# Performance work log

Hardware: AMD Instinct MI355X
Metric: run time of the kernel (lower is better)

Reference implementation:

```python
import jax, jax.numpy as jnp
import numpy as np

B_SZ, L_SEQ, H_CH, N_ST = 8, 4096, 256, 64


def setup_inputs() -> dict:
    key = jax.random.key(0)
    ks = jax.random.split(key, 12)
    rn = lambda k, s, sc=1.0: jax.random.normal(k, s, jnp.float32) * sc
    inp = {
        'x': rn(ks[0], (B_SZ, L_SEQ, H_CH)),
        # stable DPLR spectrum: Re(Lambda) < 0, HiPPO-like imaginary ladder
        'Lambda_re': -(jnp.abs(rn(ks[1], (N_ST,))) + 0.1),
        'Lambda_im': jnp.pi * jnp.arange(N_ST, dtype=jnp.float32),
        'P_re': rn(ks[2], (N_ST,), N_ST ** -0.5),
        'P_im': rn(ks[3], (N_ST,), N_ST ** -0.5),
        'Q_re': rn(ks[4], (N_ST,), N_ST ** -0.5),
        'Q_im': rn(ks[5], (N_ST,), N_ST ** -0.5),
        'B_re': rn(ks[6], (N_ST,), N_ST ** -0.5),
        'B_im': rn(ks[7], (N_ST,), N_ST ** -0.5),
        'C_re': rn(ks[8], (H_CH, N_ST), N_ST ** -0.5),
        'C_im': rn(ks[9], (H_CH, N_ST), N_ST ** -0.5),
        'step': jnp.ones((1,), jnp.float32) * 1e-3,
        'D': jnp.zeros((1,), jnp.float32),
        'W_fc': rn(ks[10], (H_CH, H_CH), H_CH ** -0.5),
        'b_fc': jnp.zeros((H_CH,), jnp.float32),
        'ln_g': jnp.ones((H_CH,), jnp.float32),
        'ln_b': jnp.zeros((H_CH,), jnp.float32),
    }
    return inp


def _dplr_kernel(Lambda_re, Lambda_im, P_re, P_im, Q_re, Q_im, B_re, B_im, C_re, C_im, step, L):
    # S4 DPLR generating function evaluated at the L roots of unity (torch_get_K_derta).
    Lam = (Lambda_re + 1j * Lambda_im).astype(jnp.complex64)  # (N,)
    Pc = (P_re + 1j * P_im).astype(jnp.complex64)
    Qc = (Q_re + 1j * Q_im).astype(jnp.complex64)
    Bc = (B_re + 1j * B_im).astype(jnp.complex64)
    Cc = (C_re + 1j * C_im).astype(jnp.complex64)  # (H, N)
    k = jnp.arange(L, dtype=jnp.float32)
    Omega = jnp.exp((-2j * jnp.pi) * (k / L)).astype(jnp.complex64)  # (L,)
    c = 2.0 / (1.0 + Omega)
    g = (2.0 / step[0]) * (1.0 - Omega) / (1.0 + Omega)  # bilinear transform points, (L,)
    inv = 1.0 / (g[:, None] - Lam[None, :])  # Cauchy matrix, (L, N)
    k00 = jnp.einsum('hn,ln->hl', Cc * Bc[None, :], inv)  # (H, L)
    k01 = jnp.einsum('hn,ln->hl', Cc * Pc[None, :], inv)
    k10 = jnp.einsum('n,ln->l', Qc * Bc, inv)  # (L,)
    k11 = jnp.einsum('n,ln->l', Qc * Pc, inv)
    atRoots = c[None, :] * (k00 - k01 * (k10 / (1.0 + k11))[None, :])  # Woodbury correction
    K = jnp.fft.ifft(atRoots, axis=-1).real  # (H, L)
    return K.astype(jnp.float32)


def reference(x, Lambda_re, Lambda_im, P_re, P_im, Q_re, Q_im, B_re, B_im, C_re, C_im, step, D, W_fc, b_fc, ln_g, ln_b):
    Bsz, L, H = x.shape
    step = jnp.maximum(step, 1e-6)
    K = _dplr_kernel(Lambda_re, Lambda_im, P_re, P_im, Q_re, Q_im, B_re, B_im, C_re, C_im, step, L)  # (H, L)
    # causal FFT convolution per channel (torch_convolution with fft=True)
    n = 2 * L
    Kf = jnp.fft.rfft(K, n=n, axis=-1)           # (H, F)
    uf = jnp.fft.rfft(x, n=n, axis=1)            # (B, F, H)
    h1 = jnp.fft.irfft(uf * Kf.T[None], n=n, axis=1)[:, :L, :]
    y1 = jax.nn.gelu(h1 + D * x, approximate=False)  # mult_activation='gelu'
    y2 = jax.nn.gelu(y1 @ W_fc.T + b_fc, approximate=False)  # fc + final_act
    y2 = y2 + x  # skip
    mu = jnp.mean(y2, axis=-1, keepdims=True)
    var = jnp.var(y2, axis=-1, keepdims=True)
    y = (y2 - mu) / jnp.sqrt(var + 1e-5) * ln_g + ln_b  # LayerNorm; dropout p=0
    h_ratio = jnp.max(jnp.abs(y), axis=1) / (jnp.max(jnp.abs(x), axis=1) + 1e-6)  # (B, H)
    return y, h_ratio
```

## Files before the change

### kernel.cpp

```cpp
#include <hip/hip_runtime.h>
#include <math.h>

#define TPB 256

typedef float2 cf;
typedef __attribute__((ext_vector_type(8))) short bf16x8;
typedef __attribute__((ext_vector_type(4))) float f32x4;

__device__ __forceinline__ cf cmk(float x, float y){ cf r; r.x=x; r.y=y; return r; }
__device__ __forceinline__ cf cml(cf a, cf b){ return cmk(a.x*b.x - a.y*b.y, a.x*b.y + a.y*b.x); }
__device__ __forceinline__ cf cad(cf a, cf b){ return cmk(a.x+b.x, a.y+b.y); }
__device__ __forceinline__ cf csb(cf a, cf b){ return cmk(a.x-b.x, a.y-b.y); }
__device__ __forceinline__ cf crcp(cf d){ float r = 1.0f/(d.x*d.x + d.y*d.y); return cmk(d.x*r, -d.y*r); }
__device__ __forceinline__ cf cdv(cf n, cf d){ return cml(n, crcp(d)); }
__device__ __forceinline__ float geluf(float z){ return 0.5f*z*(1.0f + erff(z*0.70710678118654752f)); }

__device__ __forceinline__ cf twid(float f, float sign){
  float h = f * 0.5f;
  float s = __builtin_amdgcn_sinf(h);
  float c0 = __builtin_amdgcn_cosf(h);
  return cmk(c0, sign * s);
}

__device__ __forceinline__ void bfsplit(float v, ushort* h, ushort* l){
  unsigned u = __float_as_uint(v);
  unsigned hr = (u + 0x7FFFu + ((u >> 16) & 1u)) & 0xFFFF0000u;
  *h = (ushort)(hr >> 16);
  float lv = v - __uint_as_float(hr);
  unsigned u2 = __float_as_uint(lv);
  *l = (ushort)((u2 + 0x7FFFu + ((u2 >> 16) & 1u)) >> 16);
}

template<int N, int SSTART>
__device__ void fft_dif_r4(cf* __restrict__ a, float sign){
  #pragma unroll
  for (int s = SSTART; s >= 1; s >>= 2){
    __syncthreads();
    #pragma unroll
    for (int g = 0; g < (N >> 2) / TPB; g++){
      int w = (int)threadIdx.x + g * TPB;
      int j = w & (s - 1);
      int base = ((w & ~(s - 1)) << 2) | j;
      cf A0 = a[base], B0 = a[base + s], C0 = a[base + 2*s], D0 = a[base + 3*s];
      cf w1 = twid((float)j / (float)(2 * s), sign);
      cf w2 = cml(w1, w1);
      cf a1 = cad(A0, C0);
      cf c1 = cml(csb(A0, C0), w1);
      cf b1 = cad(B0, D0);
      cf d1 = cml(csb(B0, D0), cmk(-sign * w1.y, sign * w1.x));
      a[base]         = cad(a1, b1);
      a[base + s]     = cml(csb(a1, b1), w2);
      a[base + 2*s]   = cad(c1, d1);
      a[base + 3*s]   = cml(csb(c1, d1), w2);
    }
  }
  if constexpr ((__builtin_ctz(N) & 1) == 1){
    __syncthreads();
    #pragma unroll
    for (int g = 0; g < (N >> 1) / TPB; g++){
      int w = (int)threadIdx.x + g * TPB;
      int i = w << 1;
      cf u = a[i], v = a[i + 1];
      a[i] = cad(u, v);
      a[i + 1] = csb(u, v);
    }
  }
  __syncthreads();
}

template<int N>
__device__ void fft_dit_r4(cf* __restrict__ a, float sign){
  if constexpr ((__builtin_ctz(N) & 1) == 1){
    __syncthreads();
    #pragma unroll
    for (int g = 0; g < (N >> 1) / TPB; g++){
      int w = (int)threadIdx.x + g * TPB;
      int i = w << 1;
      cf u = a[i], v = a[i + 1];
      a[i] = cad(u, v);
      a[i + 1] = csb(u, v);
    }
  }
  constexpr int S0 = ((__builtin_ctz(N) & 1) == 1) ? 2 : 1;
  #pragma unroll
  for (int s = S0; s <= (N >> 2); s <<= 2){
    __syncthreads();
    #pragma unroll
    for (int g = 0; g < (N >> 2) / TPB; g++){
      int w = (int)threadIdx.x + g * TPB;
      int j = w & (s - 1);
      int base = ((w & ~(s - 1)) << 2) | j;
      cf A0 = a[base], B0 = a[base + s], C0 = a[base + 2*s], D0 = a[base + 3*s];
      cf w1 = twid((float)j / (float)(2 * s), sign);
      cf w2 = cml(w1, w1);
      cf t1 = cml(B0, w2);
      cf a1 = cad(A0, t1), b1 = csb(A0, t1);
      cf t2 = cml(D0, w2);
      cf c1 = cad(C0, t2), d1 = csb(C0, t2);
      cf v1 = cml(c1, w1);
      cf v2 = cml(d1, cmk(-sign * w1.y, sign * w1.x));
      a[base]         = cad(a1, v1);
      a[base + 2*s]   = csb(a1, v1);
      a[base + s]     = cad(b1, v2);
      a[base + 3*s]   = csb(b1, v2);
    }
  }
  __syncthreads();
}

__device__ void dif8192_pad_stage(cf* __restrict__ a, float sign){
  __syncthreads();
  #pragma unroll
  for (int g = 0; g < 8; g++){
    int w = (int)threadIdx.x + g * TPB;
    cf A0 = a[w], B0 = a[w + 2048];
    cf w1 = twid((float)w * (1.0f / 4096.0f), sign);
    cf w2 = cml(w1, w1);
    cf c1 = cml(A0, w1);
    cf d1 = cml(B0, cmk(-sign * w1.y, sign * w1.x));
    a[w]        = cad(A0, B0);
    a[w + 2048] = cml(csb(A0, B0), w2);
    a[w + 4096] = cad(c1, d1);
    a[w + 6144] = cml(csb(c1, d1), w2);
  }
}

__device__ __forceinline__ int brev13(int x){ return (int)(__brev((unsigned)x) >> 19); }

__global__ void k_init(unsigned* xmax, unsigned* ymax){
  int i = blockIdx.x * 256 + threadIdx.x;
  if (i < 2048){ xmax[i] = 0u; ymax[i] = 0u; }
}

__global__ __launch_bounds__(256) void k_transpose_x(const float* __restrict__ x,
                                                     float* __restrict__ xT,
                                                     unsigned* __restrict__ xmax){
  __shared__ float tile[64][65];
  __shared__ float red[64][4];
  int b = blockIdx.z;
  int t0 = blockIdx.x * 64;
  int h0 = blockIdx.y * 64;
  int hc = threadIdx.x & 63, tg = threadIdx.x >> 6;
  float pmax = 0.0f;
  #pragma unroll
  for (int q = 0; q < 16; q++){
    int tr = tg + q * 4;
    float v = x[((size_t)(b * 4096 + t0 + tr)) * 256 + h0 + hc];
    tile[tr][hc] = v;
    pmax = fmaxf(pmax, fabsf(v));
  }
  red[hc][tg] = pmax;
  __syncthreads();
  if (threadIdx.x < 64){
    float m = fmaxf(fmaxf(red[threadIdx.x][0], red[threadIdx.x][1]),
                    fmaxf(red[threadIdx.x][2], red[threadIdx.x][3]));
    atomicMax(&xmax[b * 256 + h0 + threadIdx.x], __float_as_uint(m));
  }
  #pragma unroll
  for (int q = 0; q < 16; q++){
    int hr = tg + q * 4;
    xT[((size_t)(b * 256 + h0 + hr)) * 4096 + t0 + hc] = tile[hc][hr];
  }
}

__global__ void k_wsplit(const float* __restrict__ W, ushort* __restrict__ Wh, ushort* __restrict__ Wl){
  int i = blockIdx.x * 256 + threadIdx.x;
  ushort h, l;
  bfsplit(W[i], &h, &l);
  Wh[i] = h; Wl[i] = l;
}

__global__ __launch_bounds__(256) void k_cauchy(
    const float* __restrict__ Lr, const float* __restrict__ Li,
    const float* __restrict__ Pr, const float* __restrict__ Pi,
    const float* __restrict__ Qr, const float* __restrict__ Qi,
    const float* __restrict__ Br, const float* __restrict__ Bi,
    const float* __restrict__ Cr, const float* __restrict__ Ci,
    const float* __restrict__ stepp, cf* __restrict__ A)
{
  __shared__ cf sLam[64], sB[64], sP[64], sQB[64], sQP[64];
  __shared__ cf sInv[64][16];
  __shared__ cf sWood[16], sC[16], sG[16];
  int tid = threadIdx.x;
  int l0 = blockIdx.x * 16;
  float stepv = fmaxf(stepp[0], 1e-6f);
  if (tid < 64){
    cf lam = cmk(Lr[tid], Li[tid]);
    cf b = cmk(Br[tid], Bi[tid]);
    cf p = cmk(Pr[tid], Pi[tid]);
    cf q = cmk(Qr[tid], Qi[tid]);
    sLam[tid] = lam; sB[tid] = b; sP[tid] = p;
    sQB[tid] = cml(q, b);
    sQP[tid] = cml(q, p);
  }
  __syncthreads();
  if (tid < 16){
    int l = l0 + tid;
    float ang = -6.2831855f * ((float)l * (1.0f / 4096.0f));
    cf Om = cmk(cosf(ang), sinf(ang));
    cf den = cmk(1.0f + Om.x, Om.y);
    cf num = cmk(1.0f - Om.x, -Om.y);
    cf rden = crcp(den);
    sC[tid] = cml(cmk(2.0f, 0.0f), rden);
    cf g = cml(num, rden);
    float sc = 2.0f / stepv;
    sG[tid] = cmk(g.x * sc, g.y * sc);
  }
  __syncthreads();
  for (int it = tid; it < 1024; it += 256){
    int n = it >> 4, ll = it & 15;
    sInv[n][ll] = crcp(csb(sG[ll], sLam[n]));
  }
  __syncthreads();
  if (tid < 16){
    cf k10 = cmk(0,0), k11 = cmk(0,0);
    for (int n = 0; n < 64; n++){
      k10 = cad(k10, cml(sQB[n], sInv[n][tid]));
      k11 = cad(k11, cml(sQP[n], sInv[n][tid]));
    }
    sWood[tid] = cdv(k10, cmk(1.0f + k11.x, k11.y));
  }
  __syncthreads();
  int h = tid;
  cf a0[16], a1[16];
  #pragma unroll
  for (int ll = 0; ll < 16; ll++){ a0[ll] = cmk(0,0); a1[ll] = cmk(0,0); }
  for (int n = 0; n < 64; n++){
    cf cc = cmk(Cr[h * 64 + n], Ci[h * 64 + n]);
    cf cb = cml(cc, sB[n]);
    cf cp = cml(cc, sP[n]);
    #pragma unroll
    for (int ll = 0; ll < 16; ll++){
      cf iv = sInv[n][ll];
      a0[ll] = cad(a0[ll], cml(cb, iv));
      a1[ll] = cad(a1[ll], cml(cp, iv));
    }
  }
  cf* dst = A + (size_t)h * 4096 + l0;
  #pragma unroll
  for (int ll = 0; ll < 16; ll++){
    dst[ll] = cml(sC[ll], csb(a0[ll], cml(a1[ll], sWood[ll])));
  }
}

__global__ __launch_bounds__(256) void k_kf(const cf* __restrict__ A, float4* __restrict__ Sab){
  extern __shared__ cf c[];
  int hp = blockIdx.x, tid = threadIdx.x;
  const cf* a1p = A + (size_t)(2 * hp) * 4096;
  const cf* a2p = a1p + 4096;
  for (int l = tid; l < 4096; l += TPB){
    int r = (int)(__brev((unsigned)l) >> 20);
    cf u = a1p[l], v = a2p[l];
    c[r] = cmk(u.x - v.y, u.y + v.x);
  }
  fft_dit_r4<4096>(c, 1.0f);
  float k1[16], k2[16];
  #pragma unroll
  for (int q = 0; q < 16; q++){
    cf w = c[tid + q * 256];
    k1[q] = w.x * (1.0f / 4096.0f);
    k2[q] = w.y * (1.0f / 4096.0f);
  }
  __syncthreads();
  #pragma unroll
  for (int q = 0; q < 16; q++) c[tid + q * 256] = cmk(k1[q], k2[q]);
  dif8192_pad_stage(c, -1.0f);
  fft_dif_r4<8192, 512>(c, -1.0f);
  float4* rec = Sab + (size_t)hp * 4097;
  const float sc = 0.5f * 0.5f * (1.0f / 8192.0f);
  #pragma unroll
  for (int q8 = 0; q8 < 16; q8++){
    int t = tid + 256 * q8;
    int p = t << 1;
    int k = brev13(p);
    int qq = brev13((8192 - k) & 8191);
    cf Zp = c[p], Zq = c[qq];
    float K1x = (Zp.x + Zq.x), K1y = (Zp.y - Zq.y);
    float dx  = (Zp.x - Zq.x), dy  = (Zp.y + Zq.y);
    float K2x = dy, K2y = -dx;
    rec[t] = make_float4((K1x + K2x) * sc, (K1y + K2y) * sc,
                         (K1x - K2x) * sc, (K1y - K2y) * sc);
  }
  if (tid == 0){
    cf Z1 = c[1];
    float K1x = 2.0f * Z1.x, K2x = 2.0f * Z1.y;
    rec[4096] = make_float4((K1x + K2x) * sc, 0.0f, (K1x - K2x) * sc, 0.0f);
  }
}

__global__ __launch_bounds__(256) void k_conv(const float* __restrict__ xT,
                                              const float4* __restrict__ Sab,
                                              const float* __restrict__ Dp,
                                              ushort* __restrict__ y1h,
                                              ushort* __restrict__ y1l){
  extern __shared__ cf c[];
  int blk = blockIdx.x;
  int b = blk >> 7, hp = blk & 127;
  int tid = threadIdx.x;
  const float* xs1 = xT + ((size_t)(b * 256 + 2 * hp)) * 4096;
  const float* xs2 = xs1 + 4096;
  for (int t = tid; t < 4096; t += TPB) c[t] = cmk(xs1[t], xs2[t]);
  dif8192_pad_stage(c, -1.0f);
  fft_dif_r4<8192, 512>(c, -1.0f);
  const float4* rec = Sab + (size_t)hp * 4097;
  #pragma unroll
  for (int q8 = 0; q8 < 16; q8++){
    int t = tid + 256 * q8;
    int p = t << 1;
    int k = brev13(p);
    int qq = brev13((8192 - k) & 8191);
    cf Zp = c[p], Zq = c[qq];
    float4 r0 = rec[t];
    cf Sap = cmk(r0.x, r0.y), Sbp = cmk(r0.z, r0.w);
    cf cZq = cmk(Zq.x, -Zq.y), cZp = cmk(Zp.x, -Zp.y);
    c[p]  = cad(cml(Zp, Sap), cml(cZq, Sbp));
    cf cSa = cmk(Sap.x, -Sap.y), cSb = cmk(Sbp.x, -Sbp.y);
    c[qq] = cad(cml(Zq, cSa), cml(cZp, cSb));
  }
  if (tid == 0){
    float4 e = rec[4096];
    cf Z1 = c[1];
    c[1] = cad(cml(Z1, cmk(e.x, e.y)), cml(cmk(Z1.x, -Z1.y), cmk(e.z, e.w)));
  }
  fft_dit_r4<8192>(c, 1.0f);
  float Dv = Dp[0];
  size_t base = ((size_t)(b * 256 + 2 * hp)) * 4096;
  for (int t = tid; t < 4096; t += TPB){
    cf w = c[t];
    float z1 = geluf(fmaf(Dv, xs1[t], w.x));
    float z2 = geluf(fmaf(Dv, xs2[t], w.y));
    ushort h0, l0, h1, l1;
    bfsplit(z1, &h0, &l0);
    bfsplit(z2, &h1, &l1);
    y1h[base + t] = h0;        y1l[base + t] = l0;
    y1h[base + 4096 + t] = h1; y1l[base + 4096 + t] = l1;
  }
}

__global__ __launch_bounds__(256, 3) void k_gemm_ln(
    const ushort* __restrict__ y1h, const ushort* __restrict__ y1l,
    const ushort* __restrict__ Wh, const ushort* __restrict__ Wl,
    const float* __restrict__ bfc, const float* __restrict__ x,
    const float* __restrict__ lng, const float* __restrict__ lnb,
    float* __restrict__ yout, unsigned* __restrict__ ymax)
{
  __shared__ ushort sY[2][64 * 40];
  __shared__ float red1[64][4], red2[64][4];
  int tid = threadIdx.x;
  int l = tid & 63;
  int w = tid >> 6;
  int blk = blockIdx.x;
  int b = blk >> 6;
  int t0 = (blk & 63) * 64;
  int g = l >> 4, cc = l & 15;

  f32x4 acc[4][4];
  #pragma unroll
  for (int m = 0; m < 4; m++)
    #pragma unroll
    for (int n = 0; n < 4; n++)
      acc[m][n] = (f32x4){0.0f, 0.0f, 0.0f, 0.0f};

  int kk = tid >> 3, ts = (tid & 7) * 8;

  #pragma unroll 1
  for (int kc = 0; kc < 256; kc += 32){
    __syncthreads();
    {
      size_t gb = ((size_t)(b * 256 + kc + kk)) * 4096 + t0 + ts;
      float4 vh = *(const float4*)(y1h + gb);
      float4 vl = *(const float4*)(y1l + gb);
      const ushort* ph = (const ushort*)&vh;
      const ushort* pl = (const ushort*)&vl;
      int kblk = kk >> 3, kin = kk & 7;
      #pragma unroll
      for (int e = 0; e < 8; e++){
        int t = ts + e;
        int idx = t * 40 + ((kblk ^ ((t >> 3) & 3)) << 3) + kin;
        sY[0][idx] = ph[e];
        sY[1][idx] = pl[e];
      }
    }
    __syncthreads();
    bf16x8 afh[4], afl[4];
    #pragma unroll
    for (int m = 0; m < 4; m++){
      int t = m * 16 + cc;
      int idx = t * 40 + ((g ^ ((t >> 3) & 3)) << 3);
      afh[m] = *(bf16x8*)&sY[0][idx];
      afl[m] = *(bf16x8*)&sY[1][idx];
    }
    #pragma unroll
    for (int n = 0; n < 4; n++){
      size_t wj = (size_t)(w * 64 + n * 16 + cc) * 256 + kc + g * 8;
      bf16x8 bh = *(const bf16x8*)(Wh + wj);
      bf16x8 bl = *(const bf16x8*)(Wl + wj);
      #pragma unroll
      for (int m = 0; m < 4; m++){
        acc[m][n] = __builtin_amdgcn_mfma_f32_16x16x32_bf16(afh[m], bh, acc[m][n], 0, 0, 0);
        acc[m][n] = __builtin_amdgcn_mfma_f32_16x16x32_bf16(afh[m], bl, acc[m][n], 0, 0, 0);
        acc[m][n] = __builtin_amdgcn_mfma_f32_16x16x32_bf16(afl[m], bh, acc[m][n], 0, 0, 0);
      }
    }
  }

  float bj[4], gj[4], lj[4];
  #pragma unroll
  for (int n = 0; n < 4; n++){
    int j = w * 64 + n * 16 + cc;
    bj[n] = bfc[j]; gj[n] = lng[j]; lj[n] = lnb[j];
  }
  #pragma unroll
  for (int m = 0; m < 4; m++){
    #pragma unroll
    for (int r = 0; r < 4; r++){
      int tl = m * 16 + g * 4 + r;
      size_t rowb = ((size_t)(b * 4096 + t0 + tl)) * 256;
      float ss = 0.0f, sq = 0.0f;
      #pragma unroll
      for (int n = 0; n < 4; n++){
        float z = geluf(acc[m][n][r] + bj[n]) + x[rowb + w * 64 + n * 16 + cc];
        acc[m][n][r] = z;
        ss += z; sq = fmaf(z, z, sq);
      }
      #pragma unroll
      for (int msk = 1; msk < 16; msk <<= 1){
        ss += __shfl_xor(ss, msk);
        sq += __shfl_xor(sq, msk);
      }
      if (cc == 0){ red1[tl][w] = ss; red2[tl][w] = sq; }
    }
  }
  __syncthreads();
  float jm[4] = {0.0f, 0.0f, 0.0f, 0.0f};
  #pragma unroll
  for (int m = 0; m < 4; m++){
    #pragma unroll
    for (int r = 0; r < 4; r++){
      int tl = m * 16 + g * 4 + r;
      float ts1 = red1[tl][0] + red1[tl][1] + red1[tl][2] + red1[tl][3];
      float ts2 = red2[tl][0] + red2[tl][1] + red2[tl][2] + red2[tl][3];
      float mu = ts1 * (1.0f / 256.0f);
      float var = ts2 * (1.0f / 256.0f) - mu * mu;
      float rstd = rsqrtf(var + 1e-5f);
      size_t rowb = ((size_t)(b * 4096 + t0 + tl)) * 256;
      #pragma unroll
      for (int n = 0; n < 4; n++){
        float yv = (acc[m][n][r] - mu) * rstd * gj[n] + lj[n];
        yout[rowb + w * 64 + n * 16 + cc] = yv;
        jm[n] = fmaxf(jm[n], fabsf(yv));
      }
    }
  }
  #pragma unroll
  for (int n = 0; n < 4; n++){
    jm[n] = fmaxf(jm[n], __shfl_xor(jm[n], 16));
    jm[n] = fmaxf(jm[n], __shfl_xor(jm[n], 32));
  }
  if (g == 0){
    #pragma unroll
    for (int n = 0; n < 4; n++)
      atomicMax(&ymax[b * 256 + w * 64 + n * 16 + cc], __float_as_uint(jm[n]));
  }
}

__global__ void k_ratio(const unsigned* __restrict__ ymax, const unsigned* __restrict__ xmax,
                        float* __restrict__ out){
  int i = blockIdx.x * 256 + threadIdx.x;
  if (i < 2048){
    float ym = __uint_as_float(ymax[i]);
    float xm = __uint_as_float(xmax[i]);
    out[8388608 + i] = ym / (xm + 1e-6f);
  }
}

extern "C" void kernel_launch(void* const* d_in, const int* in_sizes, int n_in,
                              void* d_out, int out_size, void* d_ws, size_t ws_size,
                              hipStream_t stream)
{
  const float* x    = (const float*)d_in[0];
  const float* Lr   = (const float*)d_in[1];
  const float* Li   = (const float*)d_in[2];
  const float* Pr   = (const float*)d_in[3];
  const float* Pi   = (const float*)d_in[4];
  const float* Qr   = (const float*)d_in[5];
  const float* Qi   = (const float*)d_in[6];
  const float* Br   = (const float*)d_in[7];
  const float* Bi   = (const float*)d_in[8];
  const float* Cr   = (const float*)d_in[9];
  const float* Ci   = (const float*)d_in[10];
  const float* stp  = (const float*)d_in[11];
  const float* Dp   = (const float*)d_in[12];
  const float* Wfc  = (const float*)d_in[13];
  const float* bfc  = (const float*)d_in[14];
  const float* lng  = (const float*)d_in[15];
  const float* lnb  = (const float*)d_in[16];

  char* ws = (char*)d_ws;
  float*    xT   = (float*)(ws);
  float4*   Sab  = (float4*)(ws + ((size_t)32 << 20));
  cf*       A    = (cf*)(ws + ((size_t)41 << 20));
  ushort*   y1h  = (ushort*)(ws + ((size_t)41 << 20));
  ushort*   y1l  = (ushort*)(ws + ((size_t)57 << 20));
  ushort*   Wh   = (ushort*)(ws + ((size_t)73 << 20));
  ushort*   Wl   = (ushort*)(ws + ((size_t)73 << 20) + (128u << 10));
  unsigned* xmax = (unsigned*)(ws + ((size_t)73 << 20) + (256u << 10));
  unsigned* ymax = xmax + 2048;

  k_init<<<8, 256, 0, stream>>>(xmax, ymax);
  dim3 gt(64, 4, 8);
  k_transpose_x<<<gt, 256, 0, stream>>>(x, xT, xmax);
  k_wsplit<<<256, 256, 0, stream>>>(Wfc, Wh, Wl);
  k_cauchy<<<256, 256, 0, stream>>>(Lr, Li, Pr, Pi, Qr, Qi, Br, Bi, Cr, Ci, stp, A);
  k_kf<<<128, 256, 65536, stream>>>(A, Sab);
  k_conv<<<1024, 256, 65536, stream>>>(xT, Sab, Dp, y1h, y1l);
  k_gemm_ln<<<512, 256, 0, stream>>>(y1h, y1l, Wh, Wl, bfc, x, lng, lnb, (float*)d_out, ymax);
  k_ratio<<<8, 256, 0, stream>>>(ymax, xmax, (float*)d_out);
}
```

Measured before the change: 215.4 us.

## Register-resident 8192-point FFT in k_conv with shuffle stages and padded LDS

Result: no change. 211.2 us (-2.0%).

```diff
diff --git a/kernel.cpp b/kernel.cpp
--- a/kernel.cpp
+++ b/kernel.cpp
@@ -22,6 +22,10 @@
   return cmk(c0, sign * s);
 }
 
+__device__ __forceinline__ cf shflx(cf v, int m){
+  return cmk(__shfl_xor(v.x, m), __shfl_xor(v.y, m));
+}
+
 __device__ __forceinline__ void bfsplit(float v, ushort* h, ushort* l){
   unsigned u = __float_as_uint(v);
   unsigned hr = (u + 0x7FFFu + ((u >> 16) & 1u)) & 0xFFFF0000u;
@@ -29,6 +33,31 @@
   float lv = v - __uint_as_float(hr);
   unsigned u2 = __float_as_uint(lv);
   *l = (ushort)((u2 + 0x7FFFu + ((u2 >> 16) & 1u)) >> 16);
+}
+
+__device__ __forceinline__ void dif4q(cf& q0, cf& q1, cf& q2, cf& q3, cf w1, float sign){
+  cf w2 = cml(w1, w1);
+  cf a1 = cad(q0, q2);
+  cf c1 = cml(csb(q0, q2), w1);
+  cf b1 = cad(q1, q3);
+  cf d1 = cml(csb(q1, q3), cmk(-sign*w1.y, sign*w1.x));
+  q0 = cad(a1, b1);
+  q1 = cml(csb(a1, b1), w2);
+  q2 = cad(c1, d1);
+  q3 = cml(csb(c1, d1), w2);
+}
+__device__ __forceinline__ void dit4q(cf& q0, cf& q1, cf& q2, cf& q3, cf w1, float sign){
+  cf w2 = cml(w1, w1);
+  cf t1 = cml(q1, w2);
+  cf a1 = cad(q0, t1), b1 = csb(q0, t1);
+  cf t2 = cml(q3, w2);
+  cf c1 = cad(q2, t2), d1 = csb(q2, t2);
+  cf v1 = cml(c1, w1);
+  cf v2 = cml(d1, cmk(-sign*w1.y, sign*w1.x));
+  q0 = cad(a1, v1);
+  q2 = csb(a1, v1);
+  q1 = cad(b1, v2);
+  q3 = csb(b1, v2);
 }
 
 template<int N, int SSTART>
@@ -293,47 +322,196 @@
                                               const float* __restrict__ Dp,
                                               ushort* __restrict__ y1h,
                                               ushort* __restrict__ y1l){
-  extern __shared__ cf c[];
+  __shared__ cf c[8320];
   int blk = blockIdx.x;
   int b = blk >> 7, hp = blk & 127;
-  int tid = threadIdx.x;
+  int t = threadIdx.x;
   const float* xs1 = xT + ((size_t)(b * 256 + 2 * hp)) * 4096;
   const float* xs2 = xs1 + 4096;
-  for (int t = tid; t < 4096; t += TPB) c[t] = cmk(xs1[t], xs2[t]);
-  dif8192_pad_stage(c, -1.0f);
-  fft_dif_r4<8192, 512>(c, -1.0f);
+  cf v[32];
+  #pragma unroll
+  for (int r = 0; r < 16; r++){
+    int n = t + 256 * r;
+    v[r] = cmk(xs1[n], xs2[n]);
+  }
+  #pragma unroll
+  for (int r = 0; r < 16; r++)
+    v[r + 16] = cml(v[r], twid((float)(t + 256 * r) * (1.0f / 4096.0f), -1.0f));
+  #pragma unroll
+  for (int r0 = 0; r0 < 4; r0++){
+    cf w1 = twid((float)(t + 256 * r0) * (1.0f / 2048.0f), -1.0f);
+    dif4q(v[r0], v[r0 + 4], v[r0 + 8], v[r0 + 12], w1, -1.0f);
+    dif4q(v[r0 + 16], v[r0 + 20], v[r0 + 24], v[r0 + 28], w1, -1.0f);
+  }
+  {
+    cf w1 = twid((float)t * (1.0f / 512.0f), -1.0f);
+    #pragma unroll
+    for (int r = 0; r < 32; r += 4)
+      dif4q(v[r], v[r + 1], v[r + 2], v[r + 3], w1, -1.0f);
+  }
+  #pragma unroll
+  for (int r = 0; r < 32; r++) c[t + 260 * r] = v[r];
+  __syncthreads();
+  int Bq = t >> 3, sg = t & 7;
+  int m1 = Bq * 260 + sg;
+  #pragma unroll
+  for (int u = 0; u < 32; u++) v[u] = c[m1 + 8 * u];
+  #pragma unroll
+  for (int u = 0; u < 8; u++){
+    cf w1 = twid((float)(sg + 8 * u) * (1.0f / 128.0f), -1.0f);
+    dif4q(v[u], v[u + 8], v[u + 16], v[u + 24], w1, -1.0f);
+  }
+  #pragma unroll
+  for (int p2 = 0; p2 < 2; p2++){
+    cf w1 = twid((float)(sg + 8 * p2) * (1.0f / 32.0f), -1.0f);
+    #pragma unroll
+    for (int u0 = 0; u0 < 32; u0 += 8)
+      dif4q(v[u0 + p2], v[u0 + p2 + 2], v[u0 + p2 + 4], v[u0 + p2 + 6], w1, -1.0f);
+  }
+  {
+    cf tw = twid((float)sg * (1.0f / 8.0f), -1.0f);
+    #pragma unroll
+    for (int u = 0; u < 32; u += 2){
+      cf lo = cad(v[u], v[u + 1]);
+      cf hi = cml(csb(v[u], v[u + 1]), tw);
+      v[u] = lo; v[u + 1] = hi;
+    }
+  }
+  {
+    bool h4 = (sg & 4) != 0;
+    cf tw4 = twid((float)(sg & 3) * 0.25f, -1.0f);
+    #pragma unroll
+    for (int u = 0; u < 32; u++){
+      cf o = shflx(v[u], 4);
+      v[u] = h4 ? cml(csb(o, v[u]), tw4) : cad(v[u], o);
+    }
+    bool h2 = (sg & 2) != 0;
+    cf tw2 = twid((float)(sg & 1) * 0.5f, -1.0f);
+    #pragma unroll
+    for (int u = 0; u < 32; u++){
+      cf o = shflx(v[u], 2);
+      v[u] = h2 ? cml(csb(o, v[u]), tw2) : cad(v[u], o);
+    }
+    bool h1 = (sg & 1) != 0;
+    #pragma unroll
+    for (int u = 0; u < 32; u++){
+      cf o = shflx(v[u], 1);
+      v[u] = h1 ? csb(o, v[u]) : cad(v[u], o);
+    }
+  }
+  #pragma unroll
+  for (int u = 0; u < 32; u++) c[m1 + 8 * u] = v[u];
+  __syncthreads();
   const float4* rec = Sab + (size_t)hp * 4097;
   #pragma unroll
   for (int q8 = 0; q8 < 16; q8++){
-    int t = tid + 256 * q8;
-    int p = t << 1;
+    int th = t + 256 * q8;
+    int p = th << 1;
     int k = brev13(p);
     int qq = brev13((8192 - k) & 8191);
-    cf Zp = c[p], Zq = c[qq];
-    float4 r0 = rec[t];
+    int pi = p + 4 * (p >> 8), qi = qq + 4 * (qq >> 8);
+    cf Zp = c[pi], Zq = c[qi];
+    float4 r0 = rec[th];
     cf Sap = cmk(r0.x, r0.y), Sbp = cmk(r0.z, r0.w);
     cf cZq = cmk(Zq.x, -Zq.y), cZp = cmk(Zp.x, -Zp.y);
-    c[p]  = cad(cml(Zp, Sap), cml(cZq, Sbp));
+    c[pi] = cad(cml(Zp, Sap), cml(cZq, Sbp));
     cf cSa = cmk(Sap.x, -Sap.y), cSb = cmk(Sbp.x, -Sbp.y);
-    c[qq] = cad(cml(Zq, cSa), cml(cZp, cSb));
-  }
-  if (tid == 0){
+    c[qi] = cad(cml(Zq, cSa), cml(cZp, cSb));
+  }
+  if (t == 0){
     float4 e = rec[4096];
     cf Z1 = c[1];
     c[1] = cad(cml(Z1, cmk(e.x, e.y)), cml(cmk(Z1.x, -Z1.y), cmk(e.z, e.w)));
   }
-  fft_dit_r4<8192>(c, 1.0f);
+  __syncthreads();
+  #pragma unroll
+  for (int u = 0; u < 32; u++) v[u] = c[m1 + 8 * u];
+  {
+    bool h1 = (sg & 1) != 0;
+    #pragma unroll
+    for (int u = 0; u < 32; u++){
+      cf o = shflx(v[u], 1);
+      v[u] = h1 ? csb(o, v[u]) : cad(v[u], o);
+    }
+    bool h2 = (sg & 2) != 0;
+    cf w2 = twid((float)(sg & 1) * 0.5f, 1.0f);
+    #pragma unroll
+    for (int u = 0; u < 32; u++){
+      cf o = shflx(v[u], 2);
+      cf whv = cml(w2, h2 ? v[u] : o);
+      v[u] = h2 ? csb(o, whv) : cad(v[u], whv);
+    }
+    bool h4 = (sg & 4) != 0;
+    cf w4 = twid((float)(sg & 3) * 0.25f, 1.0f);
+    #pragma unroll
+    for (int u = 0; u < 32; u++){
+      cf o = shflx(v[u], 4);
+      cf whv = cml(w4, h4 ? v[u] : o);
+      v[u] = h4 ? csb(o, whv) : cad(v[u], whv);
+    }
+  }
+  {
+    cf tw = twid((float)sg * (1.0f / 8.0f), 1.0f);
+    #pragma unroll
+    for (int u = 0; u < 32; u += 2){
+      cf tb = cml(v[u + 1], tw);
+      cf a = v[u];
+      v[u] = cad(a, tb);
+      v[u + 1] = csb(a, tb);
+    }
+  }
+  #pragma unroll
+  for (int p2 = 0; p2 < 2; p2++){
+    cf w1 = twid((float)(sg + 8 * p2) * (1.0f / 32.0f), 1.0f);
+    #pragma unroll
+    for (int u0 = 0; u0 < 32; u0 += 8)
+      dit4q(v[u0 + p2], v[u0 + p2 + 2], v[u0 + p2 + 4], v[u0 + p2 + 6], w1, 1.0f);
+  }
+  #pragma unroll
+  for (int u = 0; u < 8; u++){
+    cf w1 = twid((float)(sg + 8 * u) * (1.0f / 128.0f), 1.0f);
+    dit4q(v[u], v[u + 8], v[u + 16], v[u + 24], w1, 1.0f);
+  }
+  #pragma unroll
+  for (int u = 0; u < 32; u++) c[m1 + 8 * u] = v[u];
+  __syncthreads();
+  #pragma unroll
+  for (int r = 0; r < 32; r++) v[r] = c[t + 260 * r];
+  {
+    cf tw = twid((float)t * (1.0f / 256.0f), 1.0f);
+    #pragma unroll
+    for (int r = 0; r < 32; r += 2){
+      cf tb = cml(v[r + 1], tw);
+      cf a = v[r];
+      v[r] = cad(a, tb);
+      v[r + 1] = csb(a, tb);
+    }
+  }
+  #pragma unroll
+  for (int p2 = 0; p2 < 2; p2++){
+    cf w1 = twid((float)(t + 256 * p2) * (1.0f / 1024.0f), 1.0f);
+    #pragma unroll
+    for (int r0 = 0; r0 < 32; r0 += 8)
+      dit4q(v[r0 + p2], v[r0 + p2 + 2], v[r0 + p2 + 4], v[r0 + p2 + 6], w1, 1.0f);
+  }
+  #pragma unroll
+  for (int r0 = 0; r0 < 8; r0++){
+    cf w1 = twid((float)(t + 256 * r0) * (1.0f / 4096.0f), 1.0f);
+    dit4q(v[r0], v[r0 + 8], v[r0 + 16], v[r0 + 24], w1, 1.0f);
+  }
   float Dv = Dp[0];
   size_t base = ((size_t)(b * 256 + 2 * hp)) * 4096;
-  for (int t = tid; t < 4096; t += TPB){
-    cf w = c[t];
-    float z1 = geluf(fmaf(Dv, xs1[t], w.x));
-    float z2 = geluf(fmaf(Dv, xs2[t], w.y));
-    ushort h0, l0, h1, l1;
+  #pragma unroll
+  for (int r = 0; r < 16; r++){
+    int n = t + 256 * r;
+    cf w = v[r];
+    float z1 = geluf(fmaf(Dv, xs1[n], w.x));
+    float z2 = geluf(fmaf(Dv, xs2[n], w.y));
+    ushort h0, l0, h1u, l1;
     bfsplit(z1, &h0, &l0);
-    bfsplit(z2, &h1, &l1);
-    y1h[base + t] = h0;        y1l[base + t] = l0;
-    y1h[base + 4096 + t] = h1; y1l[base + 4096 + t] = l1;
+    bfsplit(z2, &h1u, &l1);
+    y1h[base + n] = h0;        y1l[base + n] = l0;
+    y1h[base + 4096 + n] = h1u; y1l[base + 4096 + n] = l1;
   }
 }
 
@@ -513,7 +691,7 @@
   k_wsplit<<<256, 256, 0, stream>>>(Wfc, Wh, Wl);
   k_cauchy<<<256, 256, 0, stream>>>(Lr, Li, Pr, Pi, Qr, Qi, Br, Bi, Cr, Ci, stp, A);
   k_kf<<<128, 256, 65536, stream>>>(A, Sab);
-  k_conv<<<1024, 256, 65536, stream>>>(xT, Sab, Dp, y1h, y1l);
+  k_conv<<<1024, 256, 0, stream>>>(xT, Sab, Dp, y1h, y1l);
   k_gemm_ln<<<512, 256, 0, stream>>>(y1h, y1l, Wh, Wl, bfc, x, lng, lnb, (float*)d_out, ymax);
   k_ratio<<<8, 256, 0, stream>>>(ymax, xmax, (float*)d_out);
 }
```
